# Performance work log

Hardware: AMD Instinct MI355X
Metric: run time of the kernel (lower is better)

## Reference

```python
import jax, jax.numpy as jnp
import numpy as np

B, N, C = 4, 2048, 1024
H = 16
D = C // H

def setup_inputs() -> dict:
    key = jax.random.key(0)
    k1, k2, k3 = jax.random.split(key, 3)
    x = jax.random.normal(k1, (B, N, C), dtype=jnp.float32)
    qkv_w = jax.random.normal(k2, (3 * C, C), dtype=jnp.float32) * (1.0 / np.sqrt(C))
    qkv_b = jax.random.normal(k3, (3 * C,), dtype=jnp.float32) * 0.02
    return {"x": x, "qkv_w": qkv_w, "qkv_b": qkv_b}

def reference(x, qkv_w, qkv_b):
    b, n, c = x.shape
    # torch Linear: x @ W^T + b
    qkv = x @ qkv_w.T + qkv_b                      # [B,N,3C]
    qkv = qkv.reshape(b, n, 3, H, D)
    qkv = jnp.transpose(qkv, (2, 0, 3, 1, 4))       # [3,B,H,N,D]
    q, k, v = qkv[0], qkv[1], qkv[2]
    attn = jnp.einsum('bhnd,bhmd->bhnm', q, k) / jnp.sqrt(jnp.asarray(D, x.dtype))
    attn = jax.nn.softmax(attn, axis=-1)
    out = jnp.einsum('bhnm,bhmd->bhnd', attn, v)    # [B,H,N,D]
    out = jnp.transpose(out, (0, 2, 1, 3)).reshape(b, n, c)
    return out
```

## Files before the change

### kernel.cpp

```cpp
#include <hip/hip_runtime.h>
#include <hip/hip_bf16.h>

typedef __attribute__((ext_vector_type(8))) short short8;
typedef __attribute__((ext_vector_type(4))) float f32x4;
typedef __attribute__((ext_vector_type(4))) unsigned int u32x4;
typedef unsigned short u16;
typedef unsigned int u32;

typedef u32 __attribute__((address_space(1))) as1_u32;
typedef u32 __attribute__((address_space(3))) as3_u32;

#define NB 4
#define SEQ 2048
#define CH 1024
#define NH 16
#define HD 64
#define M_TOT (NB*SEQ)
#define N_TOT (3*CH)
#define K_TOT CH
#define SCL 0.18033688f

#define MFMA16(a,b,c) __builtin_amdgcn_mfma_f32_16x16x32_bf16((a),(b),(c),0,0,0)

__device__ __forceinline__ u16 f2bf(float f) {
    union { float f; u32 u; } v; v.f = f;
    u32 u = v.u;
    return (u16)((u + 0x7fffu + ((u >> 16) & 1u)) >> 16);
}

__device__ __forceinline__ u32 pkbf2(float a, float b) {
    union { __hip_bfloat162 h; u32 u; } x;
    x.h = __float22bfloat162_rn(float2{a, b});
    return x.u;
}

__global__ void cvt_bf16_kernel(const float* __restrict__ x, u16* __restrict__ xb, int nx8,
                                const float* __restrict__ w, u16* __restrict__ wb, int nw8) {
    int i = blockIdx.x * 256 + threadIdx.x;
    const float* src; u16* dst; int idx;
    if (i < nx8) { src = x; dst = xb; idx = i; }
    else { idx = i - nx8; if (idx >= nw8) return; src = w; dst = wb; }
    const float4* s4 = (const float4*)src;
    float4 a = s4[2*idx], b = s4[2*idx+1];
    u32x4 r;
    r[0] = pkbf2(a.x, a.y); r[1] = pkbf2(a.z, a.w);
    r[2] = pkbf2(b.x, b.y); r[3] = pkbf2(b.z, b.w);
    *(u32x4*)(dst + (size_t)idx*8) = r;
}

__global__ __launch_bounds__(256) void qkv_gemm_kernel(
        const u16* __restrict__ A, const u16* __restrict__ W,
        const float* __restrict__ bias,
        u16* __restrict__ qw, u16* __restrict__ kw, u16* __restrict__ vtw)
{
    __shared__ u16 As[128*32];
    __shared__ u16 Bs[128*32];
    const int t = threadIdx.x;
    const int wave = t >> 6;
    const int lane = t & 63;
    const int l15 = lane & 15, lhi = lane >> 4;
    const int wr = wave >> 1, wc = wave & 1;
    const int xcd = blockIdx.x & 7;
    const int idx = blockIdx.x >> 3;
    const int bm = xcd * 8 + (idx & 7);
    const int bn = idx >> 3;

    f32x4 acc[4][4] = {};

    const int arow = t >> 2;
    const int acol = (t & 3) * 8;
    const u16* gA = A + (size_t)(bm*128 + arow)*K_TOT + acol;
    const u16* gB = W + (size_t)(bn*128 + arow)*K_TOT + acol;

    for (int k0 = 0; k0 < K_TOT; k0 += 32) {
        #pragma unroll
        for (int i = 0; i < 2; ++i) {
            __builtin_amdgcn_global_load_lds(
                (const as1_u32*)(gA + (size_t)i*64*K_TOT + k0),
                (as3_u32*)(As + i*2048 + wave*512), 16, 0, 0);
            __builtin_amdgcn_global_load_lds(
                (const as1_u32*)(gB + (size_t)i*64*K_TOT + k0),
                (as3_u32*)(Bs + i*2048 + wave*512), 16, 0, 0);
        }
        __syncthreads();
        short8 af[4], bfr[4];
        #pragma unroll
        for (int m = 0; m < 4; ++m)
            af[m] = *(const short8*)(As + (wr*64 + m*16 + l15)*32 + lhi*8);
        #pragma unroll
        for (int n = 0; n < 4; ++n)
            bfr[n] = *(const short8*)(Bs + (wc*64 + n*16 + l15)*32 + lhi*8);
        #pragma unroll
        for (int m = 0; m < 4; ++m)
            #pragma unroll
            for (int n = 0; n < 4; ++n)
                acc[m][n] = MFMA16(af[m], bfr[n], acc[m][n]);
        __syncthreads();
    }

    const int colbase = bn*128 + wc*64;
    const int which = colbase >> 10;
    float bv[4]; int hh[4], dd[4];
    #pragma unroll
    for (int n = 0; n < 4; ++n) {
        int cg = colbase + n*16 + l15;
        bv[n] = bias[cg];
        int hd = cg & 1023;
        hh[n] = hd >> 6; dd[n] = hd & 63;
    }
    #pragma unroll
    for (int m = 0; m < 4; ++m) {
        int rowg = bm*128 + wr*64 + m*16 + lhi*4;
        #pragma unroll
        for (int j = 0; j < 4; ++j) {
            int rg = rowg + j;
            int b = rg >> 11, nseq = rg & 2047;
            #pragma unroll
            for (int n = 0; n < 4; ++n) {
                float val = acc[m][n][j] + bv[n];
                size_t bhn = (size_t)(b*NH + hh[n]);
                if (which == 0) {
                    qw[(bhn*SEQ + nseq)*HD + dd[n]] = f2bf(val * SCL);
                } else if (which == 1) {
                    kw[(bhn*SEQ + nseq)*HD + dd[n]] = f2bf(val);
                } else {
                    vtw[(bhn*HD + dd[n])*SEQ + nseq] = f2bf(val);
                }
            }
        }
    }
}

__global__ __launch_bounds__(256, 2) void attn_kernel(
        const u16* __restrict__ qw, const u16* __restrict__ kw,
        const u16* __restrict__ vtw, float* __restrict__ out)
{
    __shared__ u16 Ksh[4][64*64];
    __shared__ u16 Vsh[4][64*64];
    const int t = threadIdx.x;
    const int wave = t >> 6, lane = t & 63;
    const int l15 = lane & 15, lhi = lane >> 4;
    const int bh = blockIdx.x & 63;
    const int b = bh >> 4, h = bh & 15;
    const int q0 = (blockIdx.x >> 6) * 256 + wave * 64;

    const u16* Q  = qw  + (size_t)bh * SEQ * HD;
    const u16* Kg = kw  + (size_t)bh * SEQ * HD;
    const u16* Vg = vtw + (size_t)bh * HD * SEQ;

    const int srow = lane >> 3;
    const int scol = ((lane & 7) ^ srow) * 8;
    const int xorc = (l15 & 7) * 8;

    auto STAGE = [&](int buf, int kv) {
        #pragma unroll
        for (int half = 0; half < 2; ++half) {
            int crow = wave*16 + half*8 + srow;
            int kperm = (crow & 32) | ((crow & 12) << 1)
                      | ((crow & 16) >> 2) | (crow & 3);
            __builtin_amdgcn_global_load_lds(
                (const as1_u32*)(Kg + (size_t)(kv + kperm)*HD + scol),
                (as3_u32*)(&Ksh[buf][(wave*16 + half*8)*64]), 16, 0, 0);
            __builtin_amdgcn_global_load_lds(
                (const as1_u32*)(Vg + (size_t)crow*SEQ + kv + scol),
                (as3_u32*)(&Vsh[buf][(wave*16 + half*8)*64]), 16, 0, 0);
        }
    };

    short8 qf[4][2];
    #pragma unroll
    for (int rf = 0; rf < 4; ++rf)
        #pragma unroll
        for (int ks = 0; ks < 2; ++ks)
            qf[rf][ks] = *(const short8*)(Q + (size_t)(q0 + rf*16 + l15)*HD + ks*32 + lhi*8);

    STAGE(0, 0);
    STAGE(1, 64);
    STAGE(2, 128);

    f32x4 o[4][4] = {};
    float lpart[4] = {0.f, 0.f, 0.f, 0.f};
    u32x4 paA[4], pbA[4], paB[4], pbB[4];

#define QKSM(KBUF, PA, PB)                                                        \
    {                                                                             \
        _Pragma("unroll")                                                         \
        for (int g = 0; g < 4; ++g) {                                             \
            short8 kf0 = *(const short8*)(&(KBUF)[(g*16 + l15)*64 + ((lhi*8) ^ xorc)]);        \
            short8 kf1 = *(const short8*)(&(KBUF)[(g*16 + l15)*64 + ((32 + lhi*8) ^ xorc)]);   \
            f32x4 stg0 = {}, stg1 = {}, stg2 = {}, stg3 = {};                     \
            __builtin_amdgcn_s_setprio(1);                                        \
            stg0 = MFMA16(kf0, qf[0][0], stg0); stg1 = MFMA16(kf0, qf[1][0], stg1); \
            stg2 = MFMA16(kf0, qf[2][0], stg2); stg3 = MFMA16(kf0, qf[3][0], stg3); \
            stg0 = MFMA16(kf1, qf[0][1], stg0); stg1 = MFMA16(kf1, qf[1][1], stg1); \
            stg2 = MFMA16(kf1, qf[2][1], stg2); stg3 = MFMA16(kf1, qf[3][1], stg3); \
            __builtin_amdgcn_s_setprio(0);                                        \
            f32x4 stgs[4] = {stg0, stg1, stg2, stg3};                             \
            _Pragma("unroll")                                                     \
            for (int rf = 0; rf < 4; ++rf) {                                      \
                float p0 = __builtin_amdgcn_exp2f(stgs[rf][0]);                   \
                float p1 = __builtin_amdgcn_exp2f(stgs[rf][1]);                   \
                float p2 = __builtin_amdgcn_exp2f(stgs[rf][2]);                   \
                float p3 = __builtin_amdgcn_exp2f(stgs[rf][3]);                   \
                lpart[rf] += (p0 + p1) + (p2 + p3);                               \
                if (g < 2) {                                                      \
                    (PA)[rf][(g & 1)*2]     = pkbf2(p0, p1);                      \
                    (PA)[rf][(g & 1)*2 + 1] = pkbf2(p2, p3);                      \
                } else {                                                          \
                    (PB)[rf][(g & 1)*2]     = pkbf2(p0, p1);                      \
                    (PB)[rf][(g & 1)*2 + 1] = pkbf2(p2, p3);                      \
                }                                                                 \
            }                                                                     \
        }                                                                         \
    }

#define PVACC(VBUF, PA, PB)                                                       \
    {                                                                             \
        __builtin_amdgcn_s_setprio(1);                                            \
        _Pragma("unroll")                                                         \
        for (int ks = 0; ks < 2; ++ks)                                            \
            _Pragma("unroll")                                                     \
            for (int nd = 0; nd < 4; ++nd) {                                      \
                short8 vf = *(const short8*)(&(VBUF)[(nd*16 + l15)*64 + ((ks*32 + lhi*8) ^ xorc)]); \
                _Pragma("unroll")                                                 \
                for (int rf = 0; rf < 4; ++rf) {                                  \
                    short8 pfrag = __builtin_bit_cast(short8, ks == 0 ? (PA)[rf] : (PB)[rf]); \
                    o[rf][nd] = MFMA16(pfrag, vf, o[rf][nd]);                     \
                }                                                                 \
            }                                                                     \
        __builtin_amdgcn_s_setprio(0);                                            \
    }

#define BODY(T, BC, BN, BS, PAC, PBC, PAN, PBN)                                   \
    {                                                                             \
        asm volatile("s_waitcnt vmcnt(4)" ::: "memory");                          \
        __builtin_amdgcn_s_barrier();                                             \
        __builtin_amdgcn_sched_barrier(0);                                        \
        STAGE(BS, ((T) + 3 <= 31) ? ((T) + 3)*64 : 0);                            \
        QKSM(Ksh[BN], PAN, PBN);                                                  \
        PVACC(Vsh[BC], PAC, PBC);                                                 \
    }

    asm volatile("s_waitcnt vmcnt(8)" ::: "memory");
    __builtin_amdgcn_s_barrier();
    QKSM(Ksh[0], paA, pbA);

    for (int m = 0; m < 7; ++m) {
        int t0 = m * 4;
        BODY(t0 + 0, 0, 1, 3, paA, pbA, paB, pbB);
        BODY(t0 + 1, 1, 2, 0, paB, pbB, paA, pbA);
        BODY(t0 + 2, 2, 3, 1, paA, pbA, paB, pbB);
        BODY(t0 + 3, 3, 0, 2, paB, pbB, paA, pbA);
    }
    BODY(28, 0, 1, 3, paA, pbA, paB, pbB);
    BODY(29, 1, 2, 0, paB, pbB, paA, pbA);
    BODY(30, 2, 3, 1, paA, pbA, paB, pbB);
    PVACC(Vsh[3], paB, pbB);

#undef BODY
#undef PVACC
#undef QKSM

    #pragma unroll
    for (int rf = 0; rf < 4; ++rf) {
        float l = lpart[rf];
        l += __shfl_xor(l, 16);
        l += __shfl_xor(l, 32);
        #pragma unroll
        for (int j = 0; j < 4; ++j) {
            float inv = 1.0f / __shfl(l, lhi*4 + j);
            int qrow = q0 + rf*16 + lhi*4 + j;
            float* orow = out + ((size_t)(b*SEQ + qrow))*CH + h*HD;
            #pragma unroll
            for (int nd = 0; nd < 4; ++nd)
                orow[nd*16 + l15] = o[rf][nd][j] * inv;
        }
    }
}

extern "C" void kernel_launch(void* const* d_in, const int* in_sizes, int n_in,
                              void* d_out, int out_size, void* d_ws, size_t ws_size,
                              hipStream_t stream) {
    const float* x    = (const float*)d_in[0];
    const float* w    = (const float*)d_in[1];
    const float* bias = (const float*)d_in[2];
    float* out = (float*)d_out;

    const size_t BHND = (size_t)NB*NH*SEQ*HD;
    u16* qw  = (u16*)d_ws;
    u16* kw  = qw  + BHND;
    u16* vtw = kw  + BHND;
    u16* xbf = vtw + BHND;
    u16* wbf = xbf + (size_t)M_TOT*K_TOT;

    const int nx8 = M_TOT*K_TOT/8;
    const int nw8 = N_TOT*K_TOT/8;
    cvt_bf16_kernel<<<(nx8+nw8+255)/256, 256, 0, stream>>>(x, xbf, nx8, w, wbf, nw8);
    qkv_gemm_kernel<<<(M_TOT/128)*(N_TOT/128), 256, 0, stream>>>(xbf, wbf, bias, qw, kw, vtw);
    attn_kernel<<<(SEQ/256)*NB*NH, 256, 0, stream>>>(qw, kw, vtw, out);
}
```

Before: 195.4 us.

## Split attention block across eight waves with 32 query rows each

The attention kernel now launches 512 threads per block, and each of the eight waves handles 32 query rows instead of 64. K/V tile staging is divided across the eight waves, one load per wave per tile, and the vmcnt thresholds are adjusted to match. The aim is more waves in flight and lower register pressure per wave, to better hide latency. In exchange, each K/V fragment read from LDS feeds fewer MFMAs, so LDS traffic per FLOP doubles, and barrier synchronisation spans more waves.

```diff
diff --git a/kernel.cpp b/kernel.cpp
--- a/kernel.cpp
+++ b/kernel.cpp
@@ -131,7 +131,7 @@
     }
 }
 
-__global__ __launch_bounds__(256, 2) void attn_kernel(
+__global__ __launch_bounds__(512, 2) void attn_kernel(
         const u16* __restrict__ qw, const u16* __restrict__ kw,
         const u16* __restrict__ vtw, float* __restrict__ out)
 {
@@ -142,7 +142,7 @@
     const int l15 = lane & 15, lhi = lane >> 4;
     const int bh = blockIdx.x & 63;
     const int b = bh >> 4, h = bh & 15;
-    const int q0 = (blockIdx.x >> 6) * 256 + wave * 64;
+    const int q0 = (blockIdx.x >> 6) * 256 + wave * 32;
 
     const u16* Q  = qw  + (size_t)bh * SEQ * HD;
     const u16* Kg = kw  + (size_t)bh * SEQ * HD;
@@ -150,26 +150,23 @@
 
     const int srow = lane >> 3;
     const int scol = ((lane & 7) ^ srow) * 8;
+    const int crow = wave * 8 + srow;
+    const int kperm = (crow & 32) | ((crow & 12) << 1)
+                    | ((crow & 16) >> 2) | (crow & 3);
     const int xorc = (l15 & 7) * 8;
 
     auto STAGE = [&](int buf, int kv) {
-        #pragma unroll
-        for (int half = 0; half < 2; ++half) {
-            int crow = wave*16 + half*8 + srow;
-            int kperm = (crow & 32) | ((crow & 12) << 1)
-                      | ((crow & 16) >> 2) | (crow & 3);
-            __builtin_amdgcn_global_load_lds(
-                (const as1_u32*)(Kg + (size_t)(kv + kperm)*HD + scol),
-                (as3_u32*)(&Ksh[buf][(wave*16 + half*8)*64]), 16, 0, 0);
-            __builtin_amdgcn_global_load_lds(
-                (const as1_u32*)(Vg + (size_t)crow*SEQ + kv + scol),
-                (as3_u32*)(&Vsh[buf][(wave*16 + half*8)*64]), 16, 0, 0);
-        }
+        __builtin_amdgcn_global_load_lds(
+            (const as1_u32*)(Kg + (size_t)(kv + kperm)*HD + scol),
+            (as3_u32*)(&Ksh[buf][wave*8*64]), 16, 0, 0);
+        __builtin_amdgcn_global_load_lds(
+            (const as1_u32*)(Vg + (size_t)crow*SEQ + kv + scol),
+            (as3_u32*)(&Vsh[buf][wave*8*64]), 16, 0, 0);
     };
 
-    short8 qf[4][2];
-    #pragma unroll
-    for (int rf = 0; rf < 4; ++rf)
+    short8 qf[2][2];
+    #pragma unroll
+    for (int rf = 0; rf < 2; ++rf)
         #pragma unroll
         for (int ks = 0; ks < 2; ++ks)
             qf[rf][ks] = *(const short8*)(Q + (size_t)(q0 + rf*16 + l15)*HD + ks*32 + lhi*8);
@@ -178,38 +175,40 @@
     STAGE(1, 64);
     STAGE(2, 128);
 
-    f32x4 o[4][4] = {};
-    float lpart[4] = {0.f, 0.f, 0.f, 0.f};
-    u32x4 paA[4], pbA[4], paB[4], pbB[4];
+    f32x4 o[2][4] = {};
+    float lpart[2] = {0.f, 0.f};
+    u32x4 paA[2], pbA[2], paB[2], pbB[2];
 
 #define QKSM(KBUF, PA, PB)                                                        \
     {                                                                             \
         _Pragma("unroll")                                                         \
         for (int g = 0; g < 4; ++g) {                                             \
-            short8 kf0 = *(const short8*)(&(KBUF)[(g*16 + l15)*64 + ((lhi*8) ^ xorc)]);        \
-            short8 kf1 = *(const short8*)(&(KBUF)[(g*16 + l15)*64 + ((32 + lhi*8) ^ xorc)]);   \
-            f32x4 stg0 = {}, stg1 = {}, stg2 = {}, stg3 = {};                     \
+            short8 kf0 = *(const short8*)(&(KBUF)[(g*16 + l15)*64 + ((lhi*8) ^ xorc)]);      \
+            short8 kf1 = *(const short8*)(&(KBUF)[(g*16 + l15)*64 + ((32 + lhi*8) ^ xorc)]); \
+            f32x4 s0 = {}, s1 = {};                                               \
             __builtin_amdgcn_s_setprio(1);                                        \
-            stg0 = MFMA16(kf0, qf[0][0], stg0); stg1 = MFMA16(kf0, qf[1][0], stg1); \
-            stg2 = MFMA16(kf0, qf[2][0], stg2); stg3 = MFMA16(kf0, qf[3][0], stg3); \
-            stg0 = MFMA16(kf1, qf[0][1], stg0); stg1 = MFMA16(kf1, qf[1][1], stg1); \
-            stg2 = MFMA16(kf1, qf[2][1], stg2); stg3 = MFMA16(kf1, qf[3][1], stg3); \
+            s0 = MFMA16(kf0, qf[0][0], s0);                                       \
+            s1 = MFMA16(kf0, qf[1][0], s1);                                       \
+            s0 = MFMA16(kf1, qf[0][1], s0);                                       \
+            s1 = MFMA16(kf1, qf[1][1], s1);                                       \
             __builtin_amdgcn_s_setprio(0);                                        \
-            f32x4 stgs[4] = {stg0, stg1, stg2, stg3};                             \
-            _Pragma("unroll")                                                     \
-            for (int rf = 0; rf < 4; ++rf) {                                      \
-                float p0 = __builtin_amdgcn_exp2f(stgs[rf][0]);                   \
-                float p1 = __builtin_amdgcn_exp2f(stgs[rf][1]);                   \
-                float p2 = __builtin_amdgcn_exp2f(stgs[rf][2]);                   \
-                float p3 = __builtin_amdgcn_exp2f(stgs[rf][3]);                   \
-                lpart[rf] += (p0 + p1) + (p2 + p3);                               \
-                if (g < 2) {                                                      \
-                    (PA)[rf][(g & 1)*2]     = pkbf2(p0, p1);                      \
-                    (PA)[rf][(g & 1)*2 + 1] = pkbf2(p2, p3);                      \
-                } else {                                                          \
-                    (PB)[rf][(g & 1)*2]     = pkbf2(p0, p1);                      \
-                    (PB)[rf][(g & 1)*2 + 1] = pkbf2(p2, p3);                      \
-                }                                                                 \
+            {                                                                     \
+                float p0 = __builtin_amdgcn_exp2f(s0[0]);                         \
+                float p1 = __builtin_amdgcn_exp2f(s0[1]);                         \
+                float p2 = __builtin_amdgcn_exp2f(s0[2]);                         \
+                float p3 = __builtin_amdgcn_exp2f(s0[3]);                         \
+                lpart[0] += (p0 + p1) + (p2 + p3);                                \
+                if (g < 2) { (PA)[0][(g&1)*2] = pkbf2(p0,p1); (PA)[0][(g&1)*2+1] = pkbf2(p2,p3); } \
+                else       { (PB)[0][(g&1)*2] = pkbf2(p0,p1); (PB)[0][(g&1)*2+1] = pkbf2(p2,p3); } \
+            }                                                                     \
+            {                                                                     \
+                float p0 = __builtin_amdgcn_exp2f(s1[0]);                         \
+                float p1 = __builtin_amdgcn_exp2f(s1[1]);                         \
+                float p2 = __builtin_amdgcn_exp2f(s1[2]);                         \
+                float p3 = __builtin_amdgcn_exp2f(s1[3]);                         \
+                lpart[1] += (p0 + p1) + (p2 + p3);                                \
+                if (g < 2) { (PA)[1][(g&1)*2] = pkbf2(p0,p1); (PA)[1][(g&1)*2+1] = pkbf2(p2,p3); } \
+                else       { (PB)[1][(g&1)*2] = pkbf2(p0,p1); (PB)[1][(g&1)*2+1] = pkbf2(p2,p3); } \
             }                                                                     \
         }                                                                         \
     }
@@ -222,18 +221,15 @@
             _Pragma("unroll")                                                     \
             for (int nd = 0; nd < 4; ++nd) {                                      \
                 short8 vf = *(const short8*)(&(VBUF)[(nd*16 + l15)*64 + ((ks*32 + lhi*8) ^ xorc)]); \
-                _Pragma("unroll")                                                 \
-                for (int rf = 0; rf < 4; ++rf) {                                  \
-                    short8 pfrag = __builtin_bit_cast(short8, ks == 0 ? (PA)[rf] : (PB)[rf]); \
-                    o[rf][nd] = MFMA16(pfrag, vf, o[rf][nd]);                     \
-                }                                                                 \
+                o[0][nd] = MFMA16(__builtin_bit_cast(short8, ks == 0 ? (PA)[0] : (PB)[0]), vf, o[0][nd]); \
+                o[1][nd] = MFMA16(__builtin_bit_cast(short8, ks == 0 ? (PA)[1] : (PB)[1]), vf, o[1][nd]); \
             }                                                                     \
         __builtin_amdgcn_s_setprio(0);                                            \
     }
 
 #define BODY(T, BC, BN, BS, PAC, PBC, PAN, PBN)                                   \
     {                                                                             \
-        asm volatile("s_waitcnt vmcnt(4)" ::: "memory");                          \
+        asm volatile("s_waitcnt vmcnt(2)" ::: "memory");                          \
         __builtin_amdgcn_s_barrier();                                             \
         __builtin_amdgcn_sched_barrier(0);                                        \
         STAGE(BS, ((T) + 3 <= 31) ? ((T) + 3)*64 : 0);                            \
@@ -241,12 +237,13 @@
         PVACC(Vsh[BC], PAC, PBC);                                                 \
     }
 
-    asm volatile("s_waitcnt vmcnt(8)" ::: "memory");
+    asm volatile("s_waitcnt vmcnt(4)" ::: "memory");
     __builtin_amdgcn_s_barrier();
     QKSM(Ksh[0], paA, pbA);
 
     for (int m = 0; m < 7; ++m) {
         int t0 = m * 4;
+        (void)t0;
         BODY(t0 + 0, 0, 1, 3, paA, pbA, paB, pbB);
         BODY(t0 + 1, 1, 2, 0, paB, pbB, paA, pbA);
         BODY(t0 + 2, 2, 3, 1, paA, pbA, paB, pbB);
@@ -262,7 +259,7 @@
 #undef QKSM
 
     #pragma unroll
-    for (int rf = 0; rf < 4; ++rf) {
+    for (int rf = 0; rf < 2; ++rf) {
         float l = lpart[rf];
         l += __shfl_xor(l, 16);
         l += __shfl_xor(l, 32);
@@ -297,5 +294,5 @@
     const int nw8 = N_TOT*K_TOT/8;
     cvt_bf16_kernel<<<(nx8+nw8+255)/256, 256, 0, stream>>>(x, xbf, nx8, w, wbf, nw8);
     qkv_gemm_kernel<<<(M_TOT/128)*(N_TOT/128), 256, 0, stream>>>(xbf, wbf, bias, qw, kw, vtw);
-    attn_kernel<<<(SEQ/256)*NB*NH, 256, 0, stream>>>(qw, kw, vtw, out);
-}
+    attn_kernel<<<(SEQ/256)*NB*NH, 512, 0, stream>>>(qw, kw, vtw, out);
+}
```

Measured after the change: 180.6 us. 1.08x faster.
